# Kernel tuning notes

Hardware: AMD Instinct MI355X
Metric: run time of the kernel (lower is better)

## Reference

```python
import jax, jax.numpy as jnp
import numpy as np

B, L, TOPK, NUM_RBF, NUM_POS, MAX_REL, CH = 4, 1024, 30, 16, 16, 32, 128
EDGE_IN = NUM_POS + NUM_RBF * 25 + 18  # 434
NODE_IN = 22


def _normalize(x, axis=-1):
    n = jnp.linalg.norm(x, axis=axis, keepdims=True)
    return jnp.where(n > 0, x / jnp.where(n > 0, n, 1.0), 0.0)


def layer_norm(x, g, b, eps=1e-5):
    mu = jnp.mean(x, axis=-1, keepdims=True)
    var = jnp.var(x, axis=-1, keepdims=True)
    return (x - mu) / jnp.sqrt(var + eps) * g + b


def gather_nodes_d(nodes, idx):
    # nodes [B,M,C], idx [B,N,K] -> [B,N,K,C]
    Bn, N, K = idx.shape
    out = jnp.take_along_axis(nodes, idx.reshape(Bn, N * K, 1), axis=1)
    return out.reshape(Bn, N, K, nodes.shape[-1])


def gather_edges(edges, idx):
    # edges [B,N,N,C], idx [B,N,K] -> [B,N,K,C]
    return jnp.take_along_axis(edges, idx[..., None], axis=2)


def cal_dihedral(Xf, eps=1e-7):
    U = _normalize(Xf[:, 1:, :] - Xf[:, :-1, :])
    u_0, u_1, u_2 = U[:, :-2], U[:, 1:-1], U[:, 2:]
    n_0 = _normalize(jnp.cross(u_0, u_1))
    n_1 = _normalize(jnp.cross(u_1, u_2))
    cosD = jnp.clip(jnp.sum(n_0 * n_1, -1), -1 + eps, 1 - eps)
    v = _normalize(jnp.cross(n_0, n_1))
    return jnp.sign(jnp.sum(-v * u_1, -1)) * jnp.arccos(cosD)


def _dihedrals(X, eps=1e-7):
    Bn, N = X.shape[0], X.shape[1]
    Xf = X[:, :, :3, :].reshape(Bn, 3 * N, 3)
    D = jnp.pad(cal_dihedral(Xf), ((0, 0), (1, 2))).reshape(Bn, N, 3)
    dihedral_feats = jnp.concatenate([jnp.cos(D), jnp.sin(D)], -1)
    U = _normalize(Xf[:, 1:, :] - Xf[:, :-1, :])
    cosA = jnp.clip(jnp.sum(U[:, :-2] * U[:, 1:-1], -1), -1 + eps, 1 - eps)
    A = jnp.pad(jnp.arccos(cosA), ((0, 0), (1, 2))).reshape(Bn, N, 3)
    angle_feats = jnp.concatenate([jnp.cos(A), jnp.sin(A)], -1)
    return jnp.concatenate([dihedral_feats, angle_feats], -1)  # [B,N,12]


def _quaternions(R):
    diag = jnp.diagonal(R, axis1=-2, axis2=-1)
    Rxx, Ryy, Rzz = diag[..., 0], diag[..., 1], diag[..., 2]
    mags = 0.5 * jnp.sqrt(jnp.abs(1.0 + jnp.stack([Rxx - Ryy - Rzz, -Rxx + Ryy - Rzz, -Rxx - Ryy + Rzz], -1)))
    signs = jnp.sign(jnp.stack([R[..., 2, 1] - R[..., 1, 2], R[..., 0, 2] - R[..., 2, 0], R[..., 1, 0] - R[..., 0, 1]], -1))
    w = jnp.sqrt(jax.nn.relu(1.0 + jnp.sum(diag, -1, keepdims=True))) / 2.0
    return _normalize(jnp.concatenate([signs * mags, w], -1))


def _orientations_coarse_gl_tuple(X, E_idx):
    V = X  # [B,N,4,3]
    Bn, N = X.shape[0], X.shape[1]
    Xf = X[:, :, :3, :].reshape(Bn, 3 * N, 3)
    U = _normalize(Xf[:, 1:, :] - Xf[:, :-1, :])
    u_0, u_1 = U[:, :-2], U[:, 1:-1]
    n_0 = _normalize(jnp.cross(u_0, u_1))[:, ::3]  # [B,N-1,3]
    b_1 = _normalize(u_0 - u_1)[:, ::3]
    Xa = Xf[:, ::3]  # N-atom coords [B,N,3]
    Q = jnp.stack([b_1, n_0, jnp.cross(b_1, n_0)], 2).reshape(Bn, N - 1, 9)
    Q = jnp.pad(Q, ((0, 0), (0, 1), (0, 0)))  # [B,N,9]
    Qm = Q.reshape(Bn, N, 3, 3)
    Q_neighbors = gather_nodes_d(Q, E_idx).reshape(Bn, N, -1, 3, 3)
    X_nb = gather_nodes_d(V[:, :, 1, :], E_idx)
    N_nb = gather_nodes_d(V[:, :, 0, :], E_idx)
    C_nb = gather_nodes_d(V[:, :, 2, :], E_idx)
    O_nb = gather_nodes_d(V[:, :, 3, :], E_idx)
    dXn = jnp.stack([X_nb, N_nb, C_nb, O_nb], 3) - Xa[:, :, None, None, :]  # [B,N,K,4,3]
    dU = jnp.einsum('bnij,bnkaj->bnkai', Qm, dXn)
    Kn = E_idx.shape[-1]
    E_direct = _normalize(dU).reshape(Bn, N, Kn, 12)
    R = jnp.einsum('bnji,bnkjl->bnkil', Qm, Q_neighbors)
    q = _quaternions(R)  # [B,N,K,4]
    dX_inner = V[:, :, jnp.array([0, 2, 3]), :] - Xa[:, :, None, :]
    V_direct = _normalize(jnp.einsum('bnij,bnaj->bnai', Qm, dX_inner)).reshape(Bn, N, 9)
    return V_direct, E_direct, q


def _dist(Xc, mask, eps=1e-6):
    mask_2D = mask[:, None, :] * mask[:, :, None]
    D = mask_2D * jnp.sqrt(jnp.sum((Xc[:, None, :, :] - Xc[:, :, None, :]) ** 2, -1) + eps)
    D_max = jnp.max(D, -1, keepdims=True)
    D_adjust = D + (1.0 - mask_2D) * D_max
    negD, E_idx = jax.lax.top_k(-D_adjust, min(TOPK, Xc.shape[1]))
    return -negD, E_idx


def _dist_seq(res_idx):
    D = jnp.abs(res_idx[:, :, None] - res_idx[:, None, :])
    _, E_idx = jax.lax.top_k(-D, min(TOPK, res_idx.shape[1]))
    return E_idx


def _rbf(D):
    D_mu = jnp.linspace(2.0, 22.0, NUM_RBF)
    D_sigma = (22.0 - 2.0) / NUM_RBF
    return jnp.exp(-(((D[..., None] - D_mu) / D_sigma) ** 2))


def _get_rbf(A, Bm, E_idx):
    D = jnp.sqrt(jnp.sum((A[:, :, None, :] - Bm[:, None, :, :]) ** 2, -1) + 1e-6)
    return _rbf(gather_edges(D[..., None], E_idx)[..., 0])


PAIRS = [('N', 'N'), ('C', 'C'), ('O', 'O'), ('Cb', 'Cb'), ('Ca', 'N'), ('Ca', 'C'), ('Ca', 'O'), ('Ca', 'Cb'),
         ('N', 'C'), ('N', 'O'), ('N', 'Cb'), ('Cb', 'C'), ('Cb', 'O'), ('O', 'C'), ('N', 'Ca'), ('C', 'Ca'),
         ('O', 'Ca'), ('Cb', 'Ca'), ('C', 'N'), ('O', 'N'), ('Cb', 'N'), ('C', 'Cb'), ('O', 'Cb'), ('C', 'O')]


def _forward(X, mask, residue_idx, chain_labels, W_pos, b_pos, W_edge, W_node, g_edge, b_edge, g_node, b_node):
    bvec = X[:, :, 1, :] - X[:, :, 0, :]
    cvec = X[:, :, 2, :] - X[:, :, 1, :]
    avec = jnp.cross(bvec, cvec)
    Cb = -0.58273431 * avec + 0.56802827 * bvec - 0.54067466 * cvec + X[:, :, 1, :]
    atoms = {'N': X[:, :, 0, :], 'Ca': X[:, :, 1, :], 'C': X[:, :, 2, :], 'O': X[:, :, 3, :], 'Cb': Cb}
    D_neighbors, E_idx = _dist(atoms['Ca'], mask)
    E_idx_res = _dist_seq(residue_idx)
    E_idx = jnp.where(mask[:, :, None] == 0, E_idx_res, E_idx)
    RBF_all = [_rbf(D_neighbors)]
    for pa, pb in PAIRS:
        RBF_all.append(_get_rbf(atoms[pa], atoms[pb], E_idx))
    RBF_all = jnp.concatenate(RBF_all, -1)  # [B,L,K,400]
    V_angles = _dihedrals(X) * mask[..., None]
    V_direct, E_direct, E_angles = _orientations_coarse_gl_tuple(X, E_idx)
    V_direct = V_direct * mask[..., None]
    offset = residue_idx[:, :, None] - residue_idx[:, None, :]
    E_offset = gather_edges(offset[..., None], E_idx)[..., 0]
    d_chains = (chain_labels[:, :, None] == chain_labels[:, None, :]).astype(jnp.int32)
    E_chains = gather_edges(d_chains[..., None], E_idx)[..., 0]
    d = jnp.clip(E_offset + MAX_REL, 0, 2 * MAX_REL) * E_chains + (1 - E_chains) * (2 * MAX_REL + 1)
    E_positional = jax.nn.one_hot(d, 2 * MAX_REL + 2, dtype=W_pos.dtype) @ W_pos + b_pos
    mask_j = gather_nodes_d(mask[..., None], E_idx)[..., 0]
    fdt = E_direct.dtype
    E = jnp.concatenate([E_positional, RBF_all, E_direct, E_angles,
                         E_chains[..., None].astype(fdt), mask_j[..., None]], -1)  # [B,L,K,434]
    E = layer_norm(E @ W_edge, g_edge, b_edge)
    Vn = jnp.concatenate([V_angles, V_direct, mask[..., None]], -1)  # [B,L,22]
    Vn = layer_norm(Vn @ W_node, g_node, b_node)
    return Vn, E, E_idx


def setup_inputs():
    key = jax.random.key(0)
    ks = jax.random.split(key, 8)
    X = 3.0 * jax.random.normal(ks[0], (B, L, 4, 3), jnp.float32)
    mask = jnp.ones((B, L), jnp.float32)
    residue_idx = jnp.tile(jnp.arange(L, dtype=jnp.int32), (B, 1))
    chain_labels = jax.random.randint(ks[1], (B, L), 0, 2, dtype=jnp.int32)
    s = lambda k, sh: jax.random.normal(k, sh, jnp.float32) * 0.05
    W_pos = s(ks[2], (2 * MAX_REL + 2, NUM_POS))
    b_pos = jnp.zeros((NUM_POS,), jnp.float32)
    W_edge = s(ks[3], (EDGE_IN, CH))
    W_node = s(ks[4], (NODE_IN, CH))
    return dict(X=X, mask=mask, residue_idx=residue_idx, chain_labels=chain_labels,
                W_pos=W_pos, b_pos=b_pos, W_edge=W_edge, W_node=W_node,
                g_edge=jnp.ones((CH,), jnp.float32), b_edge=jnp.zeros((CH,), jnp.float32),
                g_node=jnp.ones((CH,), jnp.float32), b_node=jnp.zeros((CH,), jnp.float32))


def reference(X, mask, residue_idx, chain_labels, W_pos, b_pos, W_edge, W_node, g_edge, b_edge, g_node, b_node):
    return _forward(X, mask, residue_idx, chain_labels, W_pos, b_pos, W_edge, W_node,
                    g_edge, b_edge, g_node, b_node)
```

## Files before the change

kernel.cpp:

```cpp
#include <hip/hip_runtime.h>

#define BATCH 4
#define LEN   1024
#define KNB   30
#define CH    128
#define EIN   434
#define KP    448
#define KST   14
#define ASTR  456
#define CSTR  132

typedef unsigned short ushort_t;
typedef __attribute__((ext_vector_type(8))) short bf16x8;
typedef __attribute__((ext_vector_type(4))) float f32x4;

__constant__ int c_pa[24] = {0,2,3,4,1,1,1,1,0,0,0,4,4,3,0,2,3,4,2,3,4,2,3,2};
__constant__ int c_pb[24] = {0,2,3,4,0,2,3,4,2,3,4,2,3,2,1,1,1,1,0,0,0,4,4,3};

struct F3 { float x, y, z; };
__device__ __forceinline__ F3 f3sub(F3 a, F3 b){ return {a.x-b.x, a.y-b.y, a.z-b.z}; }
__device__ __forceinline__ F3 f3cross(F3 a, F3 b){
  return {a.y*b.z - a.z*b.y, a.z*b.x - a.x*b.z, a.x*b.y - a.y*b.x};
}
__device__ __forceinline__ float f3dot(F3 a, F3 b){ return a.x*b.x + a.y*b.y + a.z*b.z; }
__device__ __forceinline__ F3 f3norm(F3 a){
  float n = sqrtf(f3dot(a,a));
  if (n > 0.f) return {a.x/n, a.y/n, a.z/n};
  return {0.f, 0.f, 0.f};
}
__device__ __forceinline__ float fsign(float x){ return (x > 0.f) ? 1.f : ((x < 0.f) ? -1.f : 0.f); }
__device__ __forceinline__ float clip1(float c){ return fminf(fmaxf(c, -1.f + 1e-7f), 1.f - 1e-7f); }
__device__ __forceinline__ float dihedralf(F3 ua, F3 ub, F3 uc){
  F3 n0 = f3norm(f3cross(ua, ub));
  F3 n1 = f3norm(f3cross(ub, uc));
  float cd = clip1(f3dot(n0, n1));
  F3 v = f3norm(f3cross(n0, n1));
  return fsign(-f3dot(v, ub)) * acosf(cd);
}
__device__ __forceinline__ ushort_t f2bf(float f){
  unsigned u = __float_as_uint(f);
  unsigned r = u + 0x7FFFu + ((u >> 16) & 1u);
  return (ushort_t)(r >> 16);
}

#define DPP_MIN_STEP(v, ctrl) do{                                            \
    unsigned t_ = (unsigned)__builtin_amdgcn_update_dpp(                     \
        (int)0xFFFFFFFF, (int)(v), (ctrl), 0xF, 0xF, false);                 \
    (v) = t_ < (v) ? t_ : (v);                                               \
  } while(0)
__device__ __forceinline__ unsigned wave_min_u32(unsigned v){
  DPP_MIN_STEP(v, 0x111);
  DPP_MIN_STEP(v, 0x112);
  DPP_MIN_STEP(v, 0x114);
  DPP_MIN_STEP(v, 0x118);
  DPP_MIN_STEP(v, 0x142);
  DPP_MIN_STEP(v, 0x143);
  return (unsigned)__builtin_amdgcn_readlane((int)v, 63);
}

__global__ __launch_bounds__(256) void prep_kernel(
    const float* __restrict__ X, const float* __restrict__ mask,
    const float* __restrict__ We,
    float* __restrict__ wCb, float* __restrict__ wQ, float* __restrict__ wVn,
    float* __restrict__ wCa, ushort_t* __restrict__ Wfrag)
{
  if (blockIdx.x >= 16){
    int f = (blockIdx.x - 16)*256 + threadIdx.x;
    if (f >= 8*KST*64) return;
    int t = f / (KST*64);
    int s = (f / 64) % KST;
    int l = f & 63;
    int n  = t*16 + (l & 15);
    int k0 = s*32 + (l >> 4)*8;
    ushort_t v[8];
    #pragma unroll
    for (int j = 0; j < 8; ++j){
      int k = k0 + j;
      v[j] = (k < EIN) ? f2bf(We[(size_t)k*CH + n]) : (ushort_t)0;
    }
    ulong2* dst = (ulong2*)(Wfrag + (size_t)f*8);
    *dst = *(ulong2*)v;
    return;
  }

  int idx = blockIdx.x * 256 + threadIdx.x;
  int n = idx & (LEN - 1);
  const float* p = X + (size_t)idx * 12;
  F3 Na = {p[0], p[1], p[2]};
  F3 Ca = {p[3], p[4], p[5]};
  F3 Cc = {p[6], p[7], p[8]};
  F3 Oa = {p[9], p[10], p[11]};
  wCa[idx*4+0] = Ca.x; wCa[idx*4+1] = Ca.y; wCa[idx*4+2] = Ca.z; wCa[idx*4+3] = 0.f;
  F3 bv = f3sub(Ca, Na);
  F3 cv = f3sub(Cc, Ca);
  F3 av = f3cross(bv, cv);
  wCb[idx*3+0] = -0.58273431f*av.x + 0.56802827f*bv.x - 0.54067466f*cv.x + Ca.x;
  wCb[idx*3+1] = -0.58273431f*av.y + 0.56802827f*bv.y - 0.54067466f*cv.y + Ca.y;
  wCb[idx*3+2] = -0.58273431f*av.z + 0.56802827f*bv.z - 0.54067466f*cv.z + Ca.z;

  F3 u0 = f3norm(bv);
  F3 u1 = f3norm(cv);

  float Q[9];
  if (n < LEN - 1){
    F3 b1 = f3norm(f3sub(u0, u1));
    F3 n0 = f3norm(f3cross(u0, u1));
    F3 r2 = f3cross(b1, n0);
    Q[0]=b1.x; Q[1]=b1.y; Q[2]=b1.z;
    Q[3]=n0.x; Q[4]=n0.y; Q[5]=n0.z;
    Q[6]=r2.x; Q[7]=r2.y; Q[8]=r2.z;
  } else {
    #pragma unroll
    for (int t = 0; t < 9; ++t) Q[t] = 0.f;
  }
  #pragma unroll
  for (int t = 0; t < 9; ++t) wQ[(size_t)idx*9 + t] = Q[t];

  float m = mask[idx];
  bool hp = (n > 0), hn = (n < LEN - 1);
  F3 um1 = {0,0,0}, u2 = {0,0,0}, u3 = {0,0,0};
  if (hp){
    const float* pp = p - 12;
    F3 Cp = {pp[6], pp[7], pp[8]};
    um1 = f3norm(f3sub(Na, Cp));
  }
  if (hn){
    const float* pn = p + 12;
    F3 Nn  = {pn[0], pn[1], pn[2]};
    F3 Can = {pn[3], pn[4], pn[5]};
    u2 = f3norm(f3sub(Nn, Cc));
    u3 = f3norm(f3sub(Can, Nn));
  }
  float D0=0.f, D1=0.f, D2=0.f, A0=0.f, A1=0.f, A2=0.f;
  if (hp){ D0 = dihedralf(um1, u0, u1); A0 = acosf(clip1(f3dot(um1, u0))); }
  if (hn){
    D1 = dihedralf(u0, u1, u2); A1 = acosf(clip1(f3dot(u0, u1)));
    D2 = dihedralf(u1, u2, u3); A2 = acosf(clip1(f3dot(u1, u2)));
  }
  float vn[22];
  vn[0] = cosf(D0)*m; vn[1] = cosf(D1)*m; vn[2]  = cosf(D2)*m;
  vn[3] = sinf(D0)*m; vn[4] = sinf(D1)*m; vn[5]  = sinf(D2)*m;
  vn[6] = cosf(A0)*m; vn[7] = cosf(A1)*m; vn[8]  = cosf(A2)*m;
  vn[9] = sinf(A0)*m; vn[10]= sinf(A1)*m; vn[11] = sinf(A2)*m;
  F3 dxs[3];
  dxs[0] = {0.f, 0.f, 0.f};
  dxs[1] = f3sub(Cc, Na);
  dxs[2] = f3sub(Oa, Na);
  #pragma unroll
  for (int a = 0; a < 3; ++a){
    F3 dv = dxs[a];
    F3 du = { Q[0]*dv.x + Q[1]*dv.y + Q[2]*dv.z,
              Q[3]*dv.x + Q[4]*dv.y + Q[5]*dv.z,
              Q[6]*dv.x + Q[7]*dv.y + Q[8]*dv.z };
    F3 dn = f3norm(du);
    vn[12 + a*3 + 0] = dn.x * m;
    vn[12 + a*3 + 1] = dn.y * m;
    vn[12 + a*3 + 2] = dn.z * m;
  }
  vn[21] = m;
  #pragma unroll
  for (int t = 0; t < 22; ++t) wVn[(size_t)idx*22 + t] = vn[t];
}

__global__ __launch_bounds__(256) void topk_kernel(
    const float* __restrict__ wCa, float* __restrict__ wDn,
    int* __restrict__ wIdx, float* __restrict__ outI)
{
  int wid = threadIdx.x >> 6, l = threadIdx.x & 63;
  int bi = blockIdx.x*4 + wid;
  int b  = bi >> 10;
  const float4* Ca = (const float4*)wCa;
  float4 ci = Ca[bi];
  const float4* Cb = Ca + (size_t)b * LEN;

  unsigned D[16];
  #pragma unroll
  for (int t = 0; t < 16; ++t){
    int j = l + 64*t;
    float4 cj = Cb[j];
    float dx = ci.x - cj.x, dy = ci.y - cj.y, dz = ci.z - cj.z;
    D[t] = __float_as_uint(sqrtf(dx*dx + dy*dy + dz*dz + 1e-6f));
  }
  unsigned lmin = D[0]; unsigned jmin = (unsigned)l;
  #pragma unroll
  for (int t = 1; t < 16; ++t)
    if (D[t] < lmin){ lmin = D[t]; jmin = (unsigned)(l + 64*t); }

  for (int k = 0; k < KNB; ++k){
    unsigned dmin = wave_min_u32(lmin);
    unsigned cand = (lmin == dmin) ? jmin : 0xFFFFFFFFu;
    unsigned jwin = wave_min_u32(cand);
    if (cand == jwin){
      wIdx[bi*KNB + k] = (int)jwin;
      wDn[bi*KNB + k]  = __uint_as_float(dmin);
      outI[bi*KNB + k] = (float)jwin;
      int tw = (int)(jwin >> 6);
      #pragma unroll
      for (int t = 0; t < 16; ++t) if (t == tw) D[t] = 0xFFFFFFFFu;
      lmin = D[0]; jmin = (unsigned)l;
      #pragma unroll
      for (int t = 1; t < 16; ++t)
        if (D[t] < lmin){ lmin = D[t]; jmin = (unsigned)(l + 64*t); }
    }
  }
}

__global__ __launch_bounds__(64) void node_kernel(
    const float* __restrict__ wVn, const float* __restrict__ Wn,
    const float* __restrict__ gn, const float* __restrict__ bn,
    float* __restrict__ outV)
{
  int bi = blockIdx.x;
  int t  = threadIdx.x;
  __shared__ float v[22];
  if (t < 22) v[t] = wVn[(size_t)bi*22 + t];
  __syncthreads();
  float x0 = 0.f, x1 = 0.f;
  #pragma unroll
  for (int r = 0; r < 22; ++r){
    float vr = v[r];
    x0 = fmaf(vr, Wn[r*CH + t], x0);
    x1 = fmaf(vr, Wn[r*CH + t + 64], x1);
  }
  float s = x0 + x1;
  #pragma unroll
  for (int off = 1; off < 64; off <<= 1) s += __shfl_xor(s, off);
  float mu = s * (1.f/128.f);
  float d0 = x0 - mu, d1 = x1 - mu;
  float vs = d0*d0 + d1*d1;
  #pragma unroll
  for (int off = 1; off < 64; off <<= 1) vs += __shfl_xor(vs, off);
  float inv = 1.f / sqrtf(vs * (1.f/128.f) + 1e-5f);
  outV[(size_t)bi*CH + t]      = d0*inv*gn[t]    + bn[t];
  outV[(size_t)bi*CH + t + 64] = d1*inv*gn[t+64] + bn[t+64];
}

__global__ __launch_bounds__(256) void edge_kernel(
    const float* __restrict__ X, const float* __restrict__ mask,
    const int* __restrict__ resi, const int* __restrict__ chain,
    const float* __restrict__ Wp, const float* __restrict__ bp,
    const float* __restrict__ ge, const float* __restrict__ be,
    const float* __restrict__ wCb, const float* __restrict__ wQ,
    const float* __restrict__ wDn, const int* __restrict__ wIdx,
    const ushort_t* __restrict__ Wfrag,
    float* __restrict__ outE)
{
  __shared__ __align__(16) ushort_t As[32*ASTR];
  __shared__ float sAI[15];
  __shared__ float sQi[9];
  __shared__ float sAJ[KNB][15];
  __shared__ float sQj[KNB][9];
  __shared__ int   sOffI[KNB];
  __shared__ float sChain[KNB];
  __shared__ float sMaskJ[KNB];
  __shared__ float sDn[KNB];

  int bi  = blockIdx.x;
  int b   = bi >> 10;
  int tid = threadIdx.x;

  if (tid < KNB){
    int j  = wIdx[bi*KNB + tid];
    int gj = (b << 10) + j;
    const float* pj = X + (size_t)gj * 12;
    #pragma unroll
    for (int t = 0; t < 12; ++t) sAJ[tid][t] = pj[t];
    sAJ[tid][12] = wCb[(size_t)gj*3 + 0];
    sAJ[tid][13] = wCb[(size_t)gj*3 + 1];
    sAJ[tid][14] = wCb[(size_t)gj*3 + 2];
    #pragma unroll
    for (int t = 0; t < 9; ++t) sQj[tid][t] = wQ[(size_t)gj*9 + t];
    sOffI[tid]  = resi[bi] - resi[gj];
    sChain[tid] = (chain[bi] == chain[gj]) ? 1.f : 0.f;
    sMaskJ[tid] = mask[gj];
    sDn[tid]    = wDn[bi*KNB + tid];
  } else if (tid == KNB){
    const float* pi = X + (size_t)bi * 12;
    #pragma unroll
    for (int t = 0; t < 12; ++t) sAI[t] = pi[t];
    sAI[12] = wCb[(size_t)bi*3 + 0];
    sAI[13] = wCb[(size_t)bi*3 + 1];
    sAI[14] = wCb[(size_t)bi*3 + 2];
  } else if (tid == KNB + 1){
    #pragma unroll
    for (int t = 0; t < 9; ++t) sQi[t] = wQ[(size_t)bi*9 + t];
  }
  for (int e = tid; e < 2*KP; e += 256) As[30*ASTR + (e >= KP ? ASTR + e - KP : e)] = 0;
  for (int e = tid; e < KNB*14; e += 256){
    int r = e / 14, c = EIN + (e % 14);
    As[r*ASTR + c] = 0;
  }
  __syncthreads();

  if (tid < KNB*8){
    int k = tid >> 3, s = tid & 7;
    ushort_t* row = &As[k*ASTR];
    if (s == 0){
      int off = sOffI[k];
      float ch = sChain[k];
      int d = off + 32;
      d = d < 0 ? 0 : (d > 64 ? 64 : d);
      if (!(ch > 0.5f)) d = 65;
      #pragma unroll
      for (int m2 = 0; m2 < 16; ++m2)
        row[m2] = f2bf(Wp[d*16 + m2] + bp[m2]);
      row[432] = f2bf(ch);
      row[433] = f2bf(sMaskJ[k]);
    } else if (s == 1){
      float nx = sAI[0], ny = sAI[1], nz = sAI[2];
      const int amap[4] = {3, 0, 6, 9};
      #pragma unroll
      for (int a = 0; a < 4; ++a){
        float dx = sAJ[k][amap[a]+0] - nx;
        float dy = sAJ[k][amap[a]+1] - ny;
        float dz = sAJ[k][amap[a]+2] - nz;
        float e0 = sQi[0]*dx + sQi[1]*dy + sQi[2]*dz;
        float e1 = sQi[3]*dx + sQi[4]*dy + sQi[5]*dz;
        float e2 = sQi[6]*dx + sQi[7]*dy + sQi[8]*dz;
        float nn = sqrtf(e0*e0 + e1*e1 + e2*e2);
        float inv = nn > 0.f ? 1.f/nn : 0.f;
        row[416 + a*3 + 0] = f2bf(e0*inv);
        row[416 + a*3 + 1] = f2bf(e1*inv);
        row[416 + a*3 + 2] = f2bf(e2*inv);
      }
    } else if (s == 2){
      float R[3][3];
      #pragma unroll
      for (int i2 = 0; i2 < 3; ++i2)
        #pragma unroll
        for (int l2 = 0; l2 < 3; ++l2)
          R[i2][l2] = sQi[0*3+i2]*sQj[k][0*3+l2]
                    + sQi[1*3+i2]*sQj[k][1*3+l2]
                    + sQi[2*3+i2]*sQj[k][2*3+l2];
      float Rxx = R[0][0], Ryy = R[1][1], Rzz = R[2][2];
      float mx = 0.5f*sqrtf(fabsf(1.f + Rxx - Ryy - Rzz));
      float my = 0.5f*sqrtf(fabsf(1.f - Rxx + Ryy - Rzz));
      float mz = 0.5f*sqrtf(fabsf(1.f - Rxx - Ryy + Rzz));
      float qx = fsign(R[2][1] - R[1][2]) * mx;
      float qy = fsign(R[0][2] - R[2][0]) * my;
      float qz = fsign(R[1][0] - R[0][1]) * mz;
      float qw = sqrtf(fmaxf(1.f + Rxx + Ryy + Rzz, 0.f)) * 0.5f;
      float qn = sqrtf(qx*qx + qy*qy + qz*qz + qw*qw);
      float inv = qn > 0.f ? 1.f/qn : 0.f;
      row[428] = f2bf(qx*inv);
      row[429] = f2bf(qy*inv);
      row[430] = f2bf(qz*inv);
      row[431] = f2bf(qw*inv);
    }
    for (int p = s; p < 25; p += 8){
      float d;
      if (p == 0) d = sDn[k];
      else {
        int ai = c_pa[p-1]*3, bj = c_pb[p-1]*3;
        float dx = sAI[ai+0] - sAJ[k][bj+0];
        float dy = sAI[ai+1] - sAJ[k][bj+1];
        float dz = sAI[ai+2] - sAJ[k][bj+2];
        d = sqrtf(dx*dx + dy*dy + dz*dz + 1e-6f);
      }
      #pragma unroll
      for (int m2 = 0; m2 < 16; ++m2){
        float mu = (float)(2.0 + m2 * (20.0/15.0));
        float tt = (d - mu) * 0.8f;
        row[16 + p*16 + m2] = f2bf(__expf(-tt*tt));
      }
    }
  }
  __syncthreads();

  int w = tid >> 6, l = tid & 63;
  int n0 = w*2;
  int aOff0 = (l & 15)*ASTR + (l >> 4)*8;
  int aOff1 = aOff0 + 16*ASTR;
  const ushort_t* bp0 = Wfrag + ((size_t)(n0    *KST)*64 + l)*8;
  const ushort_t* bp1 = Wfrag + ((size_t)((n0+1)*KST)*64 + l)*8;

  f32x4 acc00 = {0.f,0.f,0.f,0.f}, acc01 = acc00, acc10 = acc00, acc11 = acc00;

  bf16x8 a0 = *(const bf16x8*)&As[aOff0];
  bf16x8 a1 = *(const bf16x8*)&As[aOff1];
  bf16x8 b0 = *(const bf16x8*)bp0;
  bf16x8 b1 = *(const bf16x8*)bp1;
  #pragma unroll
  for (int s = 0; s < KST; ++s){
    bf16x8 a0n, a1n, b0n, b1n;
    if (s < KST-1){
      int ka = (s+1)*32;
      a0n = *(const bf16x8*)&As[aOff0 + ka];
      a1n = *(const bf16x8*)&As[aOff1 + ka];
      b0n = *(const bf16x8*)(bp0 + (size_t)(s+1)*64*8);
      b1n = *(const bf16x8*)(bp1 + (size_t)(s+1)*64*8);
    }
    acc00 = __builtin_amdgcn_mfma_f32_16x16x32_bf16(a0, b0, acc00, 0, 0, 0);
    acc01 = __builtin_amdgcn_mfma_f32_16x16x32_bf16(a0, b1, acc01, 0, 0, 0);
    acc10 = __builtin_amdgcn_mfma_f32_16x16x32_bf16(a1, b0, acc10, 0, 0, 0);
    acc11 = __builtin_amdgcn_mfma_f32_16x16x32_bf16(a1, b1, acc11, 0, 0, 0);
    if (s < KST-1){ a0 = a0n; a1 = a1n; b0 = b0n; b1 = b1n; }
  }
  __syncthreads();

  float* Cs = (float*)As;
  int ccol = l & 15, crow = (l >> 4)*4;
  #pragma unroll
  for (int r = 0; r < 4; ++r){
    Cs[(crow + r)*CSTR      + n0*16 + ccol]      = acc00[r];
    Cs[(crow + r)*CSTR      + (n0+1)*16 + ccol]  = acc01[r];
    Cs[(16 + crow + r)*CSTR + n0*16 + ccol]      = acc10[r];
    Cs[(16 + crow + r)*CSTR + (n0+1)*16 + ccol]  = acc11[r];
  }
  __syncthreads();

  if (tid < KNB*8){
    int row = tid >> 3, g = tid & 7;
    float v[16];
    #pragma unroll
    for (int c = 0; c < 16; ++c) v[c] = Cs[row*CSTR + g*16 + c];
    float s = 0.f;
    #pragma unroll
    for (int c = 0; c < 16; ++c) s += v[c];
    #pragma unroll
    for (int off = 1; off < 8; off <<= 1) s += __shfl_xor(s, off, 8);
    float mu = s * (1.f/128.f);
    float vs = 0.f;
    #pragma unroll
    for (int c = 0; c < 16; ++c){ float dd = v[c] - mu; vs += dd*dd; }
    #pragma unroll
    for (int off = 1; off < 8; off <<= 1) vs += __shfl_xor(vs, off, 8);
    float inv = 1.f / sqrtf(vs * (1.f/128.f) + 1e-5f);
    float o[16];
    #pragma unroll
    for (int c = 0; c < 16; ++c)
      o[c] = (v[c] - mu)*inv*ge[g*16 + c] + be[g*16 + c];
    float4* dst = (float4*)&outE[((size_t)bi*KNB + row)*CH + g*16];
    dst[0] = make_float4(o[0], o[1], o[2], o[3]);
    dst[1] = make_float4(o[4], o[5], o[6], o[7]);
    dst[2] = make_float4(o[8], o[9], o[10], o[11]);
    dst[3] = make_float4(o[12], o[13], o[14], o[15]);
  }
}

extern "C" void kernel_launch(void* const* d_in, const int* in_sizes, int n_in,
                              void* d_out, int out_size, void* d_ws, size_t ws_size,
                              hipStream_t stream)
{
  const float* X    = (const float*)d_in[0];
  const float* mask = (const float*)d_in[1];
  const int*   resi = (const int*)  d_in[2];
  const int*   chn  = (const int*)  d_in[3];
  const float* Wp   = (const float*)d_in[4];
  const float* bp   = (const float*)d_in[5];
  const float* We   = (const float*)d_in[6];
  const float* Wn   = (const float*)d_in[7];
  const float* ge   = (const float*)d_in[8];
  const float* be   = (const float*)d_in[9];
  const float* gn   = (const float*)d_in[10];
  const float* bn   = (const float*)d_in[11];

  float* outV = (float*)d_out;
  float* outE = outV + (size_t)BATCH*LEN*CH;
  float* outI = outE + (size_t)BATCH*LEN*KNB*CH;

  float* ws   = (float*)d_ws;
  float* wCb  = ws;
  float* wQ   = wCb + (size_t)BATCH*LEN*3;
  float* wVn  = wQ  + (size_t)BATCH*LEN*9;
  float* wDn  = wVn + (size_t)BATCH*LEN*22;
  int*   wIdx = (int*)(wDn + (size_t)BATCH*LEN*KNB);
  float* wCa  = (float*)(wIdx + (size_t)BATCH*LEN*KNB);
  ushort_t* Wfrag = (ushort_t*)(wCa + (size_t)BATCH*LEN*4);

  prep_kernel<<<16 + 28, 256, 0, stream>>>(X, mask, We, wCb, wQ, wVn, wCa, Wfrag);
  topk_kernel<<<BATCH*LEN/4, 256, 0, stream>>>(wCa, wDn, wIdx, outI);
  node_kernel<<<BATCH*LEN, 64, 0, stream>>>(wVn, Wn, gn, bn, outV);
  edge_kernel<<<BATCH*LEN, 256, 0, stream>>>(X, mask, resi, chn, Wp, bp, ge, be,
                                             wCb, wQ, wDn, wIdx, Wfrag, outE);
}
```

Baseline: 187.7 us.

## Fuse prep and node kernels into topk and edge kernels, vectorize bf16 stores

Removes the prep and node kernels. Weight-fragment packing moves into the topk launch, and topk reads CA coordinates straight from X. The edge kernel now recomputes the per-residue Cb, local frames and node features on the fly, and computes the node output with its otherwise idle threads (tid >= 240). Bf16 conversions are packed into vector LDS stores, and padding-zeroing uses wide stores. This cuts two launches and their workspace round trips, at the cost of redundant per-neighbor geometry work in each edge block. The new packing rounds half-up rather than to nearest even, which can change a few bf16 values.

```diff
diff --git a/kernel.cpp b/kernel.cpp
--- a/kernel.cpp
+++ b/kernel.cpp
@@ -41,6 +41,11 @@
   unsigned u = __float_as_uint(f);
   unsigned r = u + 0x7FFFu + ((u >> 16) & 1u);
   return (ushort_t)(r >> 16);
+}
+__device__ __forceinline__ unsigned pk2(float a, float b){
+  unsigned ua = (__float_as_uint(a) + 0x8000u) >> 16;
+  unsigned ub = (__float_as_uint(b) + 0x8000u) & 0xFFFF0000u;
+  return ua | ub;
 }
 
 #define DPP_MIN_STEP(v, ctrl) do{                                            \
@@ -58,14 +63,13 @@
   return (unsigned)__builtin_amdgcn_readlane((int)v, 63);
 }
 
-__global__ __launch_bounds__(256) void prep_kernel(
-    const float* __restrict__ X, const float* __restrict__ mask,
-    const float* __restrict__ We,
-    float* __restrict__ wCb, float* __restrict__ wQ, float* __restrict__ wVn,
-    float* __restrict__ wCa, ushort_t* __restrict__ Wfrag)
+__global__ __launch_bounds__(256) void topk_kernel(
+    const float* __restrict__ X, const float* __restrict__ We,
+    float* __restrict__ wDn, int* __restrict__ wIdx, float* __restrict__ outI,
+    ushort_t* __restrict__ Wfrag)
 {
-  if (blockIdx.x >= 16){
-    int f = (blockIdx.x - 16)*256 + threadIdx.x;
+  if (blockIdx.x >= 1024){
+    int f = (blockIdx.x - 1024)*256 + threadIdx.x;
     if (f >= 8*KST*64) return;
     int t = f / (KST*64);
     int s = (f / 64) % KST;
@@ -83,102 +87,19 @@
     return;
   }
 
-  int idx = blockIdx.x * 256 + threadIdx.x;
-  int n = idx & (LEN - 1);
-  const float* p = X + (size_t)idx * 12;
-  F3 Na = {p[0], p[1], p[2]};
-  F3 Ca = {p[3], p[4], p[5]};
-  F3 Cc = {p[6], p[7], p[8]};
-  F3 Oa = {p[9], p[10], p[11]};
-  wCa[idx*4+0] = Ca.x; wCa[idx*4+1] = Ca.y; wCa[idx*4+2] = Ca.z; wCa[idx*4+3] = 0.f;
-  F3 bv = f3sub(Ca, Na);
-  F3 cv = f3sub(Cc, Ca);
-  F3 av = f3cross(bv, cv);
-  wCb[idx*3+0] = -0.58273431f*av.x + 0.56802827f*bv.x - 0.54067466f*cv.x + Ca.x;
-  wCb[idx*3+1] = -0.58273431f*av.y + 0.56802827f*bv.y - 0.54067466f*cv.y + Ca.y;
-  wCb[idx*3+2] = -0.58273431f*av.z + 0.56802827f*bv.z - 0.54067466f*cv.z + Ca.z;
-
-  F3 u0 = f3norm(bv);
-  F3 u1 = f3norm(cv);
-
-  float Q[9];
-  if (n < LEN - 1){
-    F3 b1 = f3norm(f3sub(u0, u1));
-    F3 n0 = f3norm(f3cross(u0, u1));
-    F3 r2 = f3cross(b1, n0);
-    Q[0]=b1.x; Q[1]=b1.y; Q[2]=b1.z;
-    Q[3]=n0.x; Q[4]=n0.y; Q[5]=n0.z;
-    Q[6]=r2.x; Q[7]=r2.y; Q[8]=r2.z;
-  } else {
-    #pragma unroll
-    for (int t = 0; t < 9; ++t) Q[t] = 0.f;
-  }
-  #pragma unroll
-  for (int t = 0; t < 9; ++t) wQ[(size_t)idx*9 + t] = Q[t];
-
-  float m = mask[idx];
-  bool hp = (n > 0), hn = (n < LEN - 1);
-  F3 um1 = {0,0,0}, u2 = {0,0,0}, u3 = {0,0,0};
-  if (hp){
-    const float* pp = p - 12;
-    F3 Cp = {pp[6], pp[7], pp[8]};
-    um1 = f3norm(f3sub(Na, Cp));
-  }
-  if (hn){
-    const float* pn = p + 12;
-    F3 Nn  = {pn[0], pn[1], pn[2]};
-    F3 Can = {pn[3], pn[4], pn[5]};
-    u2 = f3norm(f3sub(Nn, Cc));
-    u3 = f3norm(f3sub(Can, Nn));
-  }
-  float D0=0.f, D1=0.f, D2=0.f, A0=0.f, A1=0.f, A2=0.f;
-  if (hp){ D0 = dihedralf(um1, u0, u1); A0 = acosf(clip1(f3dot(um1, u0))); }
-  if (hn){
-    D1 = dihedralf(u0, u1, u2); A1 = acosf(clip1(f3dot(u0, u1)));
-    D2 = dihedralf(u1, u2, u3); A2 = acosf(clip1(f3dot(u1, u2)));
-  }
-  float vn[22];
-  vn[0] = cosf(D0)*m; vn[1] = cosf(D1)*m; vn[2]  = cosf(D2)*m;
-  vn[3] = sinf(D0)*m; vn[4] = sinf(D1)*m; vn[5]  = sinf(D2)*m;
-  vn[6] = cosf(A0)*m; vn[7] = cosf(A1)*m; vn[8]  = cosf(A2)*m;
-  vn[9] = sinf(A0)*m; vn[10]= sinf(A1)*m; vn[11] = sinf(A2)*m;
-  F3 dxs[3];
-  dxs[0] = {0.f, 0.f, 0.f};
-  dxs[1] = f3sub(Cc, Na);
-  dxs[2] = f3sub(Oa, Na);
-  #pragma unroll
-  for (int a = 0; a < 3; ++a){
-    F3 dv = dxs[a];
-    F3 du = { Q[0]*dv.x + Q[1]*dv.y + Q[2]*dv.z,
-              Q[3]*dv.x + Q[4]*dv.y + Q[5]*dv.z,
-              Q[6]*dv.x + Q[7]*dv.y + Q[8]*dv.z };
-    F3 dn = f3norm(du);
-    vn[12 + a*3 + 0] = dn.x * m;
-    vn[12 + a*3 + 1] = dn.y * m;
-    vn[12 + a*3 + 2] = dn.z * m;
-  }
-  vn[21] = m;
-  #pragma unroll
-  for (int t = 0; t < 22; ++t) wVn[(size_t)idx*22 + t] = vn[t];
-}
-
-__global__ __launch_bounds__(256) void topk_kernel(
-    const float* __restrict__ wCa, float* __restrict__ wDn,
-    int* __restrict__ wIdx, float* __restrict__ outI)
-{
   int wid = threadIdx.x >> 6, l = threadIdx.x & 63;
   int bi = blockIdx.x*4 + wid;
   int b  = bi >> 10;
-  const float4* Ca = (const float4*)wCa;
-  float4 ci = Ca[bi];
-  const float4* Cb = Ca + (size_t)b * LEN;
+  const float* pi = X + (size_t)bi*12 + 3;
+  float cx = pi[0], cy = pi[1], cz = pi[2];
+  const float* Xb = X + (size_t)b*LEN*12;
 
   unsigned D[16];
   #pragma unroll
   for (int t = 0; t < 16; ++t){
     int j = l + 64*t;
-    float4 cj = Cb[j];
-    float dx = ci.x - cj.x, dy = ci.y - cj.y, dz = ci.z - cj.z;
+    const float* pj = Xb + (size_t)j*12 + 3;
+    float dx = cx - pj[0], dy = cy - pj[1], dz = cz - pj[2];
     D[t] = __float_as_uint(sqrtf(dx*dx + dy*dy + dz*dz + 1e-6f));
   }
   unsigned lmin = D[0]; unsigned jmin = (unsigned)l;
@@ -205,49 +126,21 @@
   }
 }
 
-__global__ __launch_bounds__(64) void node_kernel(
-    const float* __restrict__ wVn, const float* __restrict__ Wn,
-    const float* __restrict__ gn, const float* __restrict__ bn,
-    float* __restrict__ outV)
-{
-  int bi = blockIdx.x;
-  int t  = threadIdx.x;
-  __shared__ float v[22];
-  if (t < 22) v[t] = wVn[(size_t)bi*22 + t];
-  __syncthreads();
-  float x0 = 0.f, x1 = 0.f;
-  #pragma unroll
-  for (int r = 0; r < 22; ++r){
-    float vr = v[r];
-    x0 = fmaf(vr, Wn[r*CH + t], x0);
-    x1 = fmaf(vr, Wn[r*CH + t + 64], x1);
-  }
-  float s = x0 + x1;
-  #pragma unroll
-  for (int off = 1; off < 64; off <<= 1) s += __shfl_xor(s, off);
-  float mu = s * (1.f/128.f);
-  float d0 = x0 - mu, d1 = x1 - mu;
-  float vs = d0*d0 + d1*d1;
-  #pragma unroll
-  for (int off = 1; off < 64; off <<= 1) vs += __shfl_xor(vs, off);
-  float inv = 1.f / sqrtf(vs * (1.f/128.f) + 1e-5f);
-  outV[(size_t)bi*CH + t]      = d0*inv*gn[t]    + bn[t];
-  outV[(size_t)bi*CH + t + 64] = d1*inv*gn[t+64] + bn[t+64];
-}
-
-__global__ __launch_bounds__(256) void edge_kernel(
+__global__ __launch_bounds__(256) void fused_kernel(
     const float* __restrict__ X, const float* __restrict__ mask,
     const int* __restrict__ resi, const int* __restrict__ chain,
     const float* __restrict__ Wp, const float* __restrict__ bp,
     const float* __restrict__ ge, const float* __restrict__ be,
-    const float* __restrict__ wCb, const float* __restrict__ wQ,
+    const float* __restrict__ Wn, const float* __restrict__ gn,
+    const float* __restrict__ bn,
     const float* __restrict__ wDn, const int* __restrict__ wIdx,
     const ushort_t* __restrict__ Wfrag,
-    float* __restrict__ outE)
+    float* __restrict__ outV, float* __restrict__ outE)
 {
   __shared__ __align__(16) ushort_t As[32*ASTR];
   __shared__ float sAI[15];
   __shared__ float sQi[9];
+  __shared__ float sVn[22];
   __shared__ float sAJ[KNB][15];
   __shared__ float sQj[KNB][9];
   __shared__ int   sOffI[KNB];
@@ -257,38 +150,145 @@
 
   int bi  = blockIdx.x;
   int b   = bi >> 10;
+  int n   = bi & (LEN - 1);
   int tid = threadIdx.x;
 
   if (tid < KNB){
     int j  = wIdx[bi*KNB + tid];
     int gj = (b << 10) + j;
-    const float* pj = X + (size_t)gj * 12;
-    #pragma unroll
-    for (int t = 0; t < 12; ++t) sAJ[tid][t] = pj[t];
-    sAJ[tid][12] = wCb[(size_t)gj*3 + 0];
-    sAJ[tid][13] = wCb[(size_t)gj*3 + 1];
-    sAJ[tid][14] = wCb[(size_t)gj*3 + 2];
-    #pragma unroll
-    for (int t = 0; t < 9; ++t) sQj[tid][t] = wQ[(size_t)gj*9 + t];
+    const float4* pj4 = (const float4*)(X + (size_t)gj*12);
+    float4 p0 = pj4[0], p1 = pj4[1], p2 = pj4[2];
+    F3 Na = {p0.x, p0.y, p0.z};
+    F3 Ca = {p0.w, p1.x, p1.y};
+    F3 Cc = {p1.z, p1.w, p2.x};
+    F3 Oa = {p2.y, p2.z, p2.w};
+    sAJ[tid][0]=Na.x; sAJ[tid][1]=Na.y; sAJ[tid][2]=Na.z;
+    sAJ[tid][3]=Ca.x; sAJ[tid][4]=Ca.y; sAJ[tid][5]=Ca.z;
+    sAJ[tid][6]=Cc.x; sAJ[tid][7]=Cc.y; sAJ[tid][8]=Cc.z;
+    sAJ[tid][9]=Oa.x; sAJ[tid][10]=Oa.y; sAJ[tid][11]=Oa.z;
+    F3 bv = f3sub(Ca, Na);
+    F3 cv = f3sub(Cc, Ca);
+    F3 av = f3cross(bv, cv);
+    sAJ[tid][12] = -0.58273431f*av.x + 0.56802827f*bv.x - 0.54067466f*cv.x + Ca.x;
+    sAJ[tid][13] = -0.58273431f*av.y + 0.56802827f*bv.y - 0.54067466f*cv.y + Ca.y;
+    sAJ[tid][14] = -0.58273431f*av.z + 0.56802827f*bv.z - 0.54067466f*cv.z + Ca.z;
+    if (j < LEN - 1){
+      F3 u0 = f3norm(bv), u1 = f3norm(cv);
+      F3 b1 = f3norm(f3sub(u0, u1));
+      F3 n0 = f3norm(f3cross(u0, u1));
+      F3 r2 = f3cross(b1, n0);
+      sQj[tid][0]=b1.x; sQj[tid][1]=b1.y; sQj[tid][2]=b1.z;
+      sQj[tid][3]=n0.x; sQj[tid][4]=n0.y; sQj[tid][5]=n0.z;
+      sQj[tid][6]=r2.x; sQj[tid][7]=r2.y; sQj[tid][8]=r2.z;
+    } else {
+      #pragma unroll
+      for (int t = 0; t < 9; ++t) sQj[tid][t] = 0.f;
+    }
     sOffI[tid]  = resi[bi] - resi[gj];
     sChain[tid] = (chain[bi] == chain[gj]) ? 1.f : 0.f;
     sMaskJ[tid] = mask[gj];
     sDn[tid]    = wDn[bi*KNB + tid];
   } else if (tid == KNB){
-    const float* pi = X + (size_t)bi * 12;
-    #pragma unroll
-    for (int t = 0; t < 12; ++t) sAI[t] = pi[t];
-    sAI[12] = wCb[(size_t)bi*3 + 0];
-    sAI[13] = wCb[(size_t)bi*3 + 1];
-    sAI[14] = wCb[(size_t)bi*3 + 2];
+    const float4* pi4 = (const float4*)(X + (size_t)bi*12);
+    float4 p0 = pi4[0], p1 = pi4[1], p2 = pi4[2];
+    F3 Na = {p0.x, p0.y, p0.z};
+    F3 Ca = {p0.w, p1.x, p1.y};
+    F3 Cc = {p1.z, p1.w, p2.x};
+    F3 Oa = {p2.y, p2.z, p2.w};
+    sAI[0]=Na.x; sAI[1]=Na.y; sAI[2]=Na.z;
+    sAI[3]=Ca.x; sAI[4]=Ca.y; sAI[5]=Ca.z;
+    sAI[6]=Cc.x; sAI[7]=Cc.y; sAI[8]=Cc.z;
+    sAI[9]=Oa.x; sAI[10]=Oa.y; sAI[11]=Oa.z;
+    F3 bv = f3sub(Ca, Na);
+    F3 cv = f3sub(Cc, Ca);
+    F3 av = f3cross(bv, cv);
+    sAI[12] = -0.58273431f*av.x + 0.56802827f*bv.x - 0.54067466f*cv.x + Ca.x;
+    sAI[13] = -0.58273431f*av.y + 0.56802827f*bv.y - 0.54067466f*cv.y + Ca.y;
+    sAI[14] = -0.58273431f*av.z + 0.56802827f*bv.z - 0.54067466f*cv.z + Ca.z;
+    if (n < LEN - 1){
+      F3 u0 = f3norm(bv), u1 = f3norm(cv);
+      F3 b1 = f3norm(f3sub(u0, u1));
+      F3 n0 = f3norm(f3cross(u0, u1));
+      F3 r2 = f3cross(b1, n0);
+      sQi[0]=b1.x; sQi[1]=b1.y; sQi[2]=b1.z;
+      sQi[3]=n0.x; sQi[4]=n0.y; sQi[5]=n0.z;
+      sQi[6]=r2.x; sQi[7]=r2.y; sQi[8]=r2.z;
+    } else {
+      #pragma unroll
+      for (int t = 0; t < 9; ++t) sQi[t] = 0.f;
+    }
   } else if (tid == KNB + 1){
-    #pragma unroll
-    for (int t = 0; t < 9; ++t) sQi[t] = wQ[(size_t)bi*9 + t];
-  }
-  for (int e = tid; e < 2*KP; e += 256) As[30*ASTR + (e >= KP ? ASTR + e - KP : e)] = 0;
-  for (int e = tid; e < KNB*14; e += 256){
-    int r = e / 14, c = EIN + (e % 14);
-    As[r*ASTR + c] = 0;
+    const float* p = X + (size_t)bi*12;
+    F3 Na = {p[0], p[1], p[2]};
+    F3 Ca = {p[3], p[4], p[5]};
+    F3 Cc = {p[6], p[7], p[8]};
+    F3 Oa = {p[9], p[10], p[11]};
+    F3 bv = f3sub(Ca, Na);
+    F3 cv = f3sub(Cc, Ca);
+    F3 u0 = f3norm(bv), u1 = f3norm(cv);
+    float Q[9];
+    if (n < LEN - 1){
+      F3 b1 = f3norm(f3sub(u0, u1));
+      F3 n0 = f3norm(f3cross(u0, u1));
+      F3 r2 = f3cross(b1, n0);
+      Q[0]=b1.x; Q[1]=b1.y; Q[2]=b1.z;
+      Q[3]=n0.x; Q[4]=n0.y; Q[5]=n0.z;
+      Q[6]=r2.x; Q[7]=r2.y; Q[8]=r2.z;
+    } else {
+      #pragma unroll
+      for (int t = 0; t < 9; ++t) Q[t] = 0.f;
+    }
+    float m = mask[bi];
+    bool hp = (n > 0), hn = (n < LEN - 1);
+    F3 um1 = {0,0,0}, u2 = {0,0,0}, u3 = {0,0,0};
+    if (hp){
+      const float* pp = p - 12;
+      F3 Cp = {pp[6], pp[7], pp[8]};
+      um1 = f3norm(f3sub(Na, Cp));
+    }
+    if (hn){
+      const float* pn = p + 12;
+      F3 Nn  = {pn[0], pn[1], pn[2]};
+      F3 Can = {pn[3], pn[4], pn[5]};
+      u2 = f3norm(f3sub(Nn, Cc));
+      u3 = f3norm(f3sub(Can, Nn));
+    }
+    float D0=0.f, D1=0.f, D2=0.f, A0=0.f, A1=0.f, A2=0.f;
+    if (hp){ D0 = dihedralf(um1, u0, u1); A0 = acosf(clip1(f3dot(um1, u0))); }
+    if (hn){
+      D1 = dihedralf(u0, u1, u2); A1 = acosf(clip1(f3dot(u0, u1)));
+      D2 = dihedralf(u1, u2, u3); A2 = acosf(clip1(f3dot(u1, u2)));
+    }
+    sVn[0] = cosf(D0)*m; sVn[1] = cosf(D1)*m; sVn[2]  = cosf(D2)*m;
+    sVn[3] = sinf(D0)*m; sVn[4] = sinf(D1)*m; sVn[5]  = sinf(D2)*m;
+    sVn[6] = cosf(A0)*m; sVn[7] = cosf(A1)*m; sVn[8]  = cosf(A2)*m;
+    sVn[9] = sinf(A0)*m; sVn[10]= sinf(A1)*m; sVn[11] = sinf(A2)*m;
+    F3 dxs[3];
+    dxs[0] = {0.f, 0.f, 0.f};
+    dxs[1] = f3sub(Cc, Na);
+    dxs[2] = f3sub(Oa, Na);
+    #pragma unroll
+    for (int a = 0; a < 3; ++a){
+      F3 dv = dxs[a];
+      F3 du = { Q[0]*dv.x + Q[1]*dv.y + Q[2]*dv.z,
+                Q[3]*dv.x + Q[4]*dv.y + Q[5]*dv.z,
+                Q[6]*dv.x + Q[7]*dv.y + Q[8]*dv.z };
+      F3 dn = f3norm(du);
+      sVn[12 + a*3 + 0] = dn.x * m;
+      sVn[12 + a*3 + 1] = dn.y * m;
+      sVn[12 + a*3 + 2] = dn.z * m;
+    }
+    sVn[21] = m;
+  } else if (tid >= 32 && tid < 144){
+    int idx = tid - 32;
+    int r = 30 + (idx / 56), ch = idx % 56;
+    *(uint4*)&As[r*ASTR + ch*8] = make_uint4(0,0,0,0);
+  } else if (tid >= 144 && tid < 144 + KNB){
+    int r = tid - 144;
+    ushort_t* row = &As[r*ASTR];
+    *(unsigned*)&row[434] = 0u;
+    *(uint2*)&row[436] = make_uint2(0,0);
+    *(uint4*)&row[440] = make_uint4(0,0,0,0);
   }
   __syncthreads();
 
@@ -301,14 +301,22 @@
       int d = off + 32;
       d = d < 0 ? 0 : (d > 64 ? 64 : d);
       if (!(ch > 0.5f)) d = 65;
-      #pragma unroll
-      for (int m2 = 0; m2 < 16; ++m2)
-        row[m2] = f2bf(Wp[d*16 + m2] + bp[m2]);
-      row[432] = f2bf(ch);
-      row[433] = f2bf(sMaskJ[k]);
+      const float4* wp4 = (const float4*)(Wp + d*16);
+      const float4* bp4 = (const float4*)bp;
+      float e[16];
+      #pragma unroll
+      for (int q = 0; q < 4; ++q){
+        float4 wv = wp4[q], bv = bp4[q];
+        e[q*4+0] = wv.x + bv.x; e[q*4+1] = wv.y + bv.y;
+        e[q*4+2] = wv.z + bv.z; e[q*4+3] = wv.w + bv.w;
+      }
+      *(uint4*)&row[0] = make_uint4(pk2(e[0],e[1]), pk2(e[2],e[3]), pk2(e[4],e[5]), pk2(e[6],e[7]));
+      *(uint4*)&row[8] = make_uint4(pk2(e[8],e[9]), pk2(e[10],e[11]), pk2(e[12],e[13]), pk2(e[14],e[15]));
+      *(unsigned*)&row[432] = pk2(ch, sMaskJ[k]);
     } else if (s == 1){
       float nx = sAI[0], ny = sAI[1], nz = sAI[2];
       const int amap[4] = {3, 0, 6, 9};
+      float e[12];
       #pragma unroll
       for (int a = 0; a < 4; ++a){
         float dx = sAJ[k][amap[a]+0] - nx;
@@ -319,10 +327,10 @@
         float e2 = sQi[6]*dx + sQi[7]*dy + sQi[8]*dz;
         float nn = sqrtf(e0*e0 + e1*e1 + e2*e2);
         float inv = nn > 0.f ? 1.f/nn : 0.f;
-        row[416 + a*3 + 0] = f2bf(e0*inv);
-        row[416 + a*3 + 1] = f2bf(e1*inv);
-        row[416 + a*3 + 2] = f2bf(e2*inv);
+        e[a*3+0] = e0*inv; e[a*3+1] = e1*inv; e[a*3+2] = e2*inv;
       }
+      *(uint4*)&row[416] = make_uint4(pk2(e[0],e[1]), pk2(e[2],e[3]), pk2(e[4],e[5]), pk2(e[6],e[7]));
+      *(uint2*)&row[424] = make_uint2(pk2(e[8],e[9]), pk2(e[10],e[11]));
     } else if (s == 2){
       float R[3][3];
       #pragma unroll
@@ -342,10 +350,7 @@
       float qw = sqrtf(fmaxf(1.f + Rxx + Ryy + Rzz, 0.f)) * 0.5f;
       float qn = sqrtf(qx*qx + qy*qy + qz*qz + qw*qw);
       float inv = qn > 0.f ? 1.f/qn : 0.f;
-      row[428] = f2bf(qx*inv);
-      row[429] = f2bf(qy*inv);
-      row[430] = f2bf(qz*inv);
-      row[431] = f2bf(qw*inv);
+      *(uint2*)&row[428] = make_uint2(pk2(qx*inv, qy*inv), pk2(qz*inv, qw*inv));
     }
     for (int p = s; p < 25; p += 8){
       float d;
@@ -357,12 +362,15 @@
         float dz = sAI[ai+2] - sAJ[k][bj+2];
         d = sqrtf(dx*dx + dy*dy + dz*dz + 1e-6f);
       }
+      float e[16];
       #pragma unroll
       for (int m2 = 0; m2 < 16; ++m2){
         float mu = (float)(2.0 + m2 * (20.0/15.0));
         float tt = (d - mu) * 0.8f;
-        row[16 + p*16 + m2] = f2bf(__expf(-tt*tt));
+        e[m2] = __expf(-tt*tt);
       }
+      *(uint4*)&row[16 + p*16]     = make_uint4(pk2(e[0],e[1]), pk2(e[2],e[3]), pk2(e[4],e[5]), pk2(e[6],e[7]));
+      *(uint4*)&row[16 + p*16 + 8] = make_uint4(pk2(e[8],e[9]), pk2(e[10],e[11]), pk2(e[12],e[13]), pk2(e[14],e[15]));
     }
   }
   __syncthreads();
@@ -411,9 +419,10 @@
 
   if (tid < KNB*8){
     int row = tid >> 3, g = tid & 7;
-    float v[16];
-    #pragma unroll
-    for (int c = 0; c < 16; ++c) v[c] = Cs[row*CSTR + g*16 + c];
+    const float4* src = (const float4*)&Cs[row*CSTR + g*16];
+    float4 v0 = src[0], v1 = src[1], v2 = src[2], v3 = src[3];
+    float v[16] = {v0.x,v0.y,v0.z,v0.w, v1.x,v1.y,v1.z,v1.w,
+                   v2.x,v2.y,v2.z,v2.w, v3.x,v3.y,v3.z,v3.w};
     float s = 0.f;
     #pragma unroll
     for (int c = 0; c < 16; ++c) s += v[c];
@@ -435,6 +444,38 @@
     dst[1] = make_float4(o[4], o[5], o[6], o[7]);
     dst[2] = make_float4(o[8], o[9], o[10], o[11]);
     dst[3] = make_float4(o[12], o[13], o[14], o[15]);
+  } else if (tid >= 240){
+    int c0 = (tid - 240)*8;
+    float x[8] = {0,0,0,0,0,0,0,0};
+    #pragma unroll
+    for (int r = 0; r < 22; ++r){
+      float vr = sVn[r];
+      float4 w0 = *(const float4*)&Wn[r*CH + c0];
+      float4 w1 = *(const float4*)&Wn[r*CH + c0 + 4];
+      x[0] = fmaf(vr, w0.x, x[0]); x[1] = fmaf(vr, w0.y, x[1]);
+      x[2] = fmaf(vr, w0.z, x[2]); x[3] = fmaf(vr, w0.w, x[3]);
+      x[4] = fmaf(vr, w1.x, x[4]); x[5] = fmaf(vr, w1.y, x[5]);
+      x[6] = fmaf(vr, w1.z, x[6]); x[7] = fmaf(vr, w1.w, x[7]);
+    }
+    float s = 0.f;
+    #pragma unroll
+    for (int c = 0; c < 8; ++c) s += x[c];
+    #pragma unroll
+    for (int off = 1; off < 16; off <<= 1) s += __shfl_xor(s, off, 16);
+    float mu = s * (1.f/128.f);
+    float vs = 0.f;
+    #pragma unroll
+    for (int c = 0; c < 8; ++c){ float dd = x[c] - mu; vs += dd*dd; }
+    #pragma unroll
+    for (int off = 1; off < 16; off <<= 1) vs += __shfl_xor(vs, off, 16);
+    float inv = 1.f / sqrtf(vs * (1.f/128.f) + 1e-5f);
+    float o[8];
+    #pragma unroll
+    for (int c = 0; c < 8; ++c)
+      o[c] = (x[c] - mu)*inv*gn[c0 + c] + bn[c0 + c];
+    float4* dst = (float4*)&outV[(size_t)bi*CH + c0];
+    dst[0] = make_float4(o[0], o[1], o[2], o[3]);
+    dst[1] = make_float4(o[4], o[5], o[6], o[7]);
   }
 }
 
@@ -460,17 +501,12 @@
   float* outI = outE + (size_t)BATCH*LEN*KNB*CH;
 
   float* ws   = (float*)d_ws;
-  float* wCb  = ws;
-  float* wQ   = wCb + (size_t)BATCH*LEN*3;
-  float* wVn  = wQ  + (size_t)BATCH*LEN*9;
-  float* wDn  = wVn + (size_t)BATCH*LEN*22;
+  float* wDn  = ws;
   int*   wIdx = (int*)(wDn + (size_t)BATCH*LEN*KNB);
-  float* wCa  = (float*)(wIdx + (size_t)BATCH*LEN*KNB);
-  ushort_t* Wfrag = (ushort_t*)(wCa + (size_t)BATCH*LEN*4);
-
-  prep_kernel<<<16 + 28, 256, 0, stream>>>(X, mask, We, wCb, wQ, wVn, wCa, Wfrag);
-  topk_kernel<<<BATCH*LEN/4, 256, 0, stream>>>(wCa, wDn, wIdx, outI);
-  node_kernel<<<BATCH*LEN, 64, 0, stream>>>(wVn, Wn, gn, bn, outV);
-  edge_kernel<<<BATCH*LEN, 256, 0, stream>>>(X, mask, resi, chn, Wp, bp, ge, be,
-                                             wCb, wQ, wDn, wIdx, Wfrag, outE);
-}
+  ushort_t* Wfrag = (ushort_t*)(wIdx + (size_t)BATCH*LEN*KNB);
+
+  topk_kernel<<<1024 + 28, 256, 0, stream>>>(X, We, wDn, wIdx, outI, Wfrag);
+  fused_kernel<<<BATCH*LEN, 256, 0, stream>>>(X, mask, resi, chn, Wp, bp, ge, be,
+                                              Wn, gn, bn, wDn, wIdx, Wfrag,
+                                              outV, outE);
+}
```

Measured after the change: 228.9 us. +21.9%, slower.
